# Optimization experiments

Hardware: AMD Instinct MI355X
Metric: run time of the kernel (lower is better)

## Reference

```python
import jax, jax.numpy as jnp
import numpy as np

NUM_ROUTING = 3  # init kwarg num_routing


def setup_inputs() -> dict:
    key = jax.random.key(0)
    k1, k2 = jax.random.split(key)
    # x: [B=128, N=1152 primary caps, C_in=8]
    x = jax.random.normal(k1, (128, 1152, 8), dtype=jnp.float32)
    # dc_w: [capsules_dim=10, num_capsules=1152, C_in=8, C_out=16]
    dc_w = jax.random.normal(k2, (10, 1152, 8, 16), dtype=jnp.float32)
    return {"x": x, "dc_w": dc_w}


def reference(x, dc_w):
    # u = x[None,:,:,None,:] @ dc_w[:,None,:,:,:]  -> [D, B, N, 1, C_out]
    u = jnp.einsum('bni,dnio->dbno', x, dc_w)[:, :, :, None, :]
    b = jnp.zeros_like(u)
    v = None
    for i in range(NUM_ROUTING):  # small fixed routing loop
        c = jax.nn.softmax(b, axis=2)                 # softmax over primary caps
        s = jnp.sum(c * u, axis=2, keepdims=True)     # [D, B, 1, 1, C_out]
        # faithful to source: norm is taken over the (singleton) axis 2,
        # so the squash coefficient is elementwise s^2 / ((1+s^2) * |s|)
        sq = s * s
        coeff = sq / ((1.0 + sq) * jnp.sqrt(sq))
        v = coeff * s
        if i != NUM_ROUTING - 1:
            b = b + jnp.sum(u * v, axis=-1, keepdims=True)  # agreement update
    return v  # [D, B, 1, 1, C_out]
```

## Files before the change

### kernel.cpp

```cpp
#include <hip/hip_runtime.h>
#include <hip/hip_bf16.h>
#include <math.h>

constexpr int NCAPS = 1152;
constexpr int CIN   = 8;
constexpr int COUT  = 16;
constexpr int BATCH = 128;
constexpr int DCAPS = 10;

__global__ __launch_bounds__(256, 1) void u_kernel(
    const float* __restrict__ x,
    const float* __restrict__ w,
    __hip_bfloat16* __restrict__ u)
{
    const int i  = blockIdx.x;
    const int bh = i & 1;
    const int nc = (i >> 1) % 72;
    const int d  = (i >> 1) / 72;

    const int t    = threadIdx.x;
    const int wv   = t >> 6;
    const int lane = t & 63;
    const int oq   = lane & 3;
    const int nl   = lane >> 2;
    const int n    = nc * 16 + nl;
    const int b0   = bh * 64 + wv * 16;

    const float* wr = w + ((size_t)(d * NCAPS + n)) * (CIN * COUT) + oq * 4;
    float4 W[CIN];
    #pragma unroll
    for (int ii = 0; ii < CIN; ++ii)
        W[ii] = *(const float4*)(wr + ii * COUT);

    const float* xp = x + ((size_t)b0 * NCAPS + n) * CIN;
    __hip_bfloat16* up = u + ((size_t)(d * BATCH + b0) * NCAPS + n) * COUT + oq * 4;

    #pragma unroll
    for (int bi = 0; bi < 16; ++bi) {
        const float4* xr = (const float4*)(xp + (size_t)bi * NCAPS * CIN);
        float4 xa = xr[0], xc = xr[1];
        float xs[CIN] = {xa.x, xa.y, xa.z, xa.w, xc.x, xc.y, xc.z, xc.w};
        float4 acc = {0.f, 0.f, 0.f, 0.f};
        #pragma unroll
        for (int ii = 0; ii < CIN; ++ii) {
            acc.x = fmaf(xs[ii], W[ii].x, acc.x);
            acc.y = fmaf(xs[ii], W[ii].y, acc.y);
            acc.z = fmaf(xs[ii], W[ii].z, acc.z);
            acc.w = fmaf(xs[ii], W[ii].w, acc.w);
        }
        union { unsigned short us[4]; uint2 v; } pk;
        pk.us[0] = __bfloat16_as_ushort(__float2bfloat16(acc.x));
        pk.us[1] = __bfloat16_as_ushort(__float2bfloat16(acc.y));
        pk.us[2] = __bfloat16_as_ushort(__float2bfloat16(acc.z));
        pk.us[3] = __bfloat16_as_ushort(__float2bfloat16(acc.w));
        *(uint2*)(up + (size_t)bi * NCAPS * COUT) = pk.v;
    }
}

constexpr int BNT  = 256;
constexpr int BWAV = BNT / 64;
constexpr int JPT  = 9;

__device__ __forceinline__ void unpack8(const uint4 pv, float* f) {
    f[0] = __uint_as_float(pv.x << 16);
    f[1] = __uint_as_float(pv.x & 0xffff0000u);
    f[2] = __uint_as_float(pv.y << 16);
    f[3] = __uint_as_float(pv.y & 0xffff0000u);
    f[4] = __uint_as_float(pv.z << 16);
    f[5] = __uint_as_float(pv.z & 0xffff0000u);
    f[6] = __uint_as_float(pv.w << 16);
    f[7] = __uint_as_float(pv.w & 0xffff0000u);
}

__global__ __launch_bounds__(BNT, 1) void routing_kernel(
    const __hip_bfloat16* __restrict__ u,
    float* __restrict__ out)
{
    __shared__ float red[BWAV][COUT];
    __shared__ float zred[BWAV];

    const int i = blockIdx.x;
    const int d = i >> 7;
    const int b = i & 127;

    const int t    = threadIdx.x;
    const int wave = t >> 6;
    const int lane = t & 63;
    const int oh   = t & 1;
    const int r    = t >> 1;

    const __hip_bfloat16* up =
        u + ((size_t)(d * BATCH + b) * NCAPS) * COUT + oh * 8;

    uint4 upk[JPT];
    #pragma unroll
    for (int j = 0; j < JPT; ++j)
        upk[j] = *(const uint4*)(up + (size_t)(j * 128 + r) * COUT);

    float bb[JPT];
    #pragma unroll
    for (int j = 0; j < JPT; ++j) bb[j] = 0.f;

    #pragma unroll
    for (int it = 0; it < 3; ++it) {
        float p8[8] = {0.f,0.f,0.f,0.f,0.f,0.f,0.f,0.f};
        float z = 0.f;
        if (it == 0) {
            #pragma unroll
            for (int j = 0; j < JPT; ++j) {
                float uf[8]; unpack8(upk[j], uf);
                #pragma unroll
                for (int k = 0; k < 8; ++k) p8[k] += uf[k];
            }
        } else {
            #pragma unroll
            for (int j = 0; j < JPT; ++j) {
                float e = __expf(bb[j] - 20.f);
                z += e;
                float uf[8]; unpack8(upk[j], uf);
                #pragma unroll
                for (int k = 0; k < 8; ++k) p8[k] = fmaf(e, uf[k], p8[k]);
            }
        }
        #pragma unroll
        for (int off = 2; off < 64; off <<= 1) {
            #pragma unroll
            for (int k = 0; k < 8; ++k) p8[k] += __shfl_xor(p8[k], off);
            if (it != 0) z += __shfl_xor(z, off);
        }
        if (lane < 2) {
            #pragma unroll
            for (int k = 0; k < 8; ++k) red[wave][oh * 8 + k] = p8[k];
            if (it != 0 && lane == 0) zred[wave] = z;
        }
        __syncthreads();

        float scale;
        if (it == 0) {
            scale = 1.f / (float)NCAPS;
        } else {
            float Z = zred[0] + zred[1] + zred[2] + zred[3];
            scale = 1.f / Z;
        }
        float vloc[8];
        #pragma unroll
        for (int k = 0; k < 8; ++k) {
            float s = red[0][oh * 8 + k] + red[1][oh * 8 + k]
                    + red[2][oh * 8 + k] + red[3][oh * 8 + k];
            s *= scale;
            vloc[k] = s * fabsf(s) / (1.f + s * s);
        }

        if (it == 2) {
            if (t < 2) {
                float* op = out + ((size_t)d * BATCH + b) * COUT + oh * 8;
                ((float4*)op)[0] = make_float4(vloc[0], vloc[1], vloc[2], vloc[3]);
                ((float4*)op)[1] = make_float4(vloc[4], vloc[5], vloc[6], vloc[7]);
            }
        } else {
            #pragma unroll
            for (int j = 0; j < JPT; ++j) {
                float uf[8]; unpack8(upk[j], uf);
                float dv = 0.f;
                #pragma unroll
                for (int k = 0; k < 8; ++k) dv = fmaf(uf[k], vloc[k], dv);
                dv += __shfl_xor(dv, 1);
                bb[j] += dv;
            }
            __syncthreads();
        }
    }
}

extern "C" void kernel_launch(void* const* d_in, const int* in_sizes, int n_in,
                              void* d_out, int out_size, void* d_ws, size_t ws_size,
                              hipStream_t stream) {
    const float* x = (const float*)d_in[0];
    const float* w = (const float*)d_in[1];
    float* out = (float*)d_out;
    __hip_bfloat16* u = (__hip_bfloat16*)d_ws;

    u_kernel<<<DCAPS * 72 * 2, 256, 0, stream>>>(x, w, u);
    routing_kernel<<<DCAPS * BATCH, BNT, 0, stream>>>(u, out);
}
```

Measured before the change: 88.95 us.

## Remap u_kernel blocks over capsules and double-buffer routing reductions

```diff
diff --git a/kernel.cpp b/kernel.cpp
--- a/kernel.cpp
+++ b/kernel.cpp
@@ -13,18 +13,18 @@
     const float* __restrict__ w,
     __hip_bfloat16* __restrict__ u)
 {
-    const int i  = blockIdx.x;
-    const int bh = i & 1;
-    const int nc = (i >> 1) % 72;
-    const int d  = (i >> 1) / 72;
+    const int i   = blockIdx.x;
+    const int bg  = i & 7;
+    const int k   = i >> 3;
+    const int nc4 = k % 18;
+    const int d   = k / 18;
 
     const int t    = threadIdx.x;
     const int wv   = t >> 6;
     const int lane = t & 63;
     const int oq   = lane & 3;
     const int nl   = lane >> 2;
-    const int n    = nc * 16 + nl;
-    const int b0   = bh * 64 + wv * 16;
+    const int n    = nc4 * 64 + wv * 16 + nl;
 
     const float* wr = w + ((size_t)(d * NCAPS + n)) * (CIN * COUT) + oq * 4;
     float4 W[CIN];
@@ -32,12 +32,13 @@
     for (int ii = 0; ii < CIN; ++ii)
         W[ii] = *(const float4*)(wr + ii * COUT);
 
-    const float* xp = x + ((size_t)b0 * NCAPS + n) * CIN;
-    __hip_bfloat16* up = u + ((size_t)(d * BATCH + b0) * NCAPS + n) * COUT + oq * 4;
+    const float* xp = x + ((size_t)bg * NCAPS + n) * CIN;
+    __hip_bfloat16* up = u + ((size_t)(d * BATCH + bg) * NCAPS + n) * COUT + oq * 4;
 
     #pragma unroll
     for (int bi = 0; bi < 16; ++bi) {
-        const float4* xr = (const float4*)(xp + (size_t)bi * NCAPS * CIN);
+        const float4* xr =
+            (const float4*)(xp + (size_t)bi * 8 * NCAPS * CIN);
         float4 xa = xr[0], xc = xr[1];
         float xs[CIN] = {xa.x, xa.y, xa.z, xa.w, xc.x, xc.y, xc.z, xc.w};
         float4 acc = {0.f, 0.f, 0.f, 0.f};
@@ -53,7 +54,7 @@
         pk.us[1] = __bfloat16_as_ushort(__float2bfloat16(acc.y));
         pk.us[2] = __bfloat16_as_ushort(__float2bfloat16(acc.z));
         pk.us[3] = __bfloat16_as_ushort(__float2bfloat16(acc.w));
-        *(uint2*)(up + (size_t)bi * NCAPS * COUT) = pk.v;
+        *(uint2*)(up + (size_t)bi * 8 * NCAPS * COUT) = pk.v;
     }
 }
 
@@ -76,8 +77,8 @@
     const __hip_bfloat16* __restrict__ u,
     float* __restrict__ out)
 {
-    __shared__ float red[BWAV][COUT];
-    __shared__ float zred[BWAV];
+    __shared__ float red[2][BWAV][COUT];
+    __shared__ float zred[2][BWAV];
 
     const int i = blockIdx.x;
     const int d = i >> 7;
@@ -97,78 +98,87 @@
     for (int j = 0; j < JPT; ++j)
         upk[j] = *(const uint4*)(up + (size_t)(j * 128 + r) * COUT);
 
+    float p8[8] = {0.f,0.f,0.f,0.f,0.f,0.f,0.f,0.f};
+    #pragma unroll
+    for (int j = 0; j < JPT; ++j) {
+        float uf[8]; unpack8(upk[j], uf);
+        #pragma unroll
+        for (int kk = 0; kk < 8; ++kk) p8[kk] += uf[kk];
+    }
+    #pragma unroll
+    for (int off = 2; off < 64; off <<= 1) {
+        #pragma unroll
+        for (int kk = 0; kk < 8; ++kk) p8[kk] += __shfl_xor(p8[kk], off);
+    }
+    if (lane < 2) {
+        #pragma unroll
+        for (int kk = 0; kk < 8; ++kk) red[0][wave][oh * 8 + kk] = p8[kk];
+    }
+    __syncthreads();
+
+    float vloc[8];
+    {
+        const float scale = 1.f / (float)NCAPS;
+        #pragma unroll
+        for (int kk = 0; kk < 8; ++kk) {
+            float s = red[0][0][oh * 8 + kk] + red[0][1][oh * 8 + kk]
+                    + red[0][2][oh * 8 + kk] + red[0][3][oh * 8 + kk];
+            s *= scale;
+            vloc[kk] = s * fabsf(s) / (1.f + s * s);
+        }
+    }
+
     float bb[JPT];
     #pragma unroll
     for (int j = 0; j < JPT; ++j) bb[j] = 0.f;
 
     #pragma unroll
-    for (int it = 0; it < 3; ++it) {
-        float p8[8] = {0.f,0.f,0.f,0.f,0.f,0.f,0.f,0.f};
+    for (int it = 1; it < 3; ++it) {
+        const int buf = it & 1;
+        float q8[8] = {0.f,0.f,0.f,0.f,0.f,0.f,0.f,0.f};
         float z = 0.f;
-        if (it == 0) {
+        #pragma unroll
+        for (int j = 0; j < JPT; ++j) {
+            float uf[8]; unpack8(upk[j], uf);
+            float dv = 0.f;
             #pragma unroll
-            for (int j = 0; j < JPT; ++j) {
-                float uf[8]; unpack8(upk[j], uf);
-                #pragma unroll
-                for (int k = 0; k < 8; ++k) p8[k] += uf[k];
-            }
-        } else {
+            for (int kk = 0; kk < 8; ++kk) dv = fmaf(uf[kk], vloc[kk], dv);
+            dv += __shfl_xor(dv, 1);
+            bb[j] += dv;
+            float e = __expf(bb[j] - 20.f);
+            z += e;
             #pragma unroll
-            for (int j = 0; j < JPT; ++j) {
-                float e = __expf(bb[j] - 20.f);
-                z += e;
-                float uf[8]; unpack8(upk[j], uf);
-                #pragma unroll
-                for (int k = 0; k < 8; ++k) p8[k] = fmaf(e, uf[k], p8[k]);
-            }
+            for (int kk = 0; kk < 8; ++kk) q8[kk] = fmaf(e, uf[kk], q8[kk]);
         }
         #pragma unroll
         for (int off = 2; off < 64; off <<= 1) {
             #pragma unroll
-            for (int k = 0; k < 8; ++k) p8[k] += __shfl_xor(p8[k], off);
-            if (it != 0) z += __shfl_xor(z, off);
+            for (int kk = 0; kk < 8; ++kk) q8[kk] += __shfl_xor(q8[kk], off);
+            z += __shfl_xor(z, off);
         }
         if (lane < 2) {
             #pragma unroll
-            for (int k = 0; k < 8; ++k) red[wave][oh * 8 + k] = p8[k];
-            if (it != 0 && lane == 0) zred[wave] = z;
+            for (int kk = 0; kk < 8; ++kk) red[buf][wave][oh * 8 + kk] = q8[kk];
+            if (lane == 0) zred[buf][wave] = z;
         }
         __syncthreads();
 
-        float scale;
-        if (it == 0) {
-            scale = 1.f / (float)NCAPS;
-        } else {
-            float Z = zred[0] + zred[1] + zred[2] + zred[3];
-            scale = 1.f / Z;
+        const float Z = zred[buf][0] + zred[buf][1]
+                      + zred[buf][2] + zred[buf][3];
+        const float scale = 1.f / Z;
+        #pragma unroll
+        for (int kk = 0; kk < 8; ++kk) {
+            float s = red[buf][0][oh * 8 + kk] + red[buf][1][oh * 8 + kk]
+                    + red[buf][2][oh * 8 + kk] + red[buf][3][oh * 8 + kk];
+            s *= scale;
+            vloc[kk] = s * fabsf(s) / (1.f + s * s);
         }
-        float vloc[8];
-        #pragma unroll
-        for (int k = 0; k < 8; ++k) {
-            float s = red[0][oh * 8 + k] + red[1][oh * 8 + k]
-                    + red[2][oh * 8 + k] + red[3][oh * 8 + k];
-            s *= scale;
-            vloc[k] = s * fabsf(s) / (1.f + s * s);
-        }
+    }
 
-        if (it == 2) {
-            if (t < 2) {
-                float* op = out + ((size_t)d * BATCH + b) * COUT + oh * 8;
-                ((float4*)op)[0] = make_float4(vloc[0], vloc[1], vloc[2], vloc[3]);
-                ((float4*)op)[1] = make_float4(vloc[4], vloc[5], vloc[6], vloc[7]);
-            }
-        } else {
-            #pragma unroll
-            for (int j = 0; j < JPT; ++j) {
-                float uf[8]; unpack8(upk[j], uf);
-                float dv = 0.f;
-                #pragma unroll
-                for (int k = 0; k < 8; ++k) dv = fmaf(uf[k], vloc[k], dv);
-                dv += __shfl_xor(dv, 1);
-                bb[j] += dv;
-            }
-            __syncthreads();
-        }
+    if (t < 2) {
+        float* op = out + ((size_t)d * BATCH + b) * COUT + oh * 8;
+        ((float4*)op)[0] = make_float4(vloc[0], vloc[1], vloc[2], vloc[3]);
+        ((float4*)op)[1] = make_float4(vloc[4], vloc[5], vloc[6], vloc[7]);
     }
 }
 
@@ -180,6 +190,6 @@
     float* out = (float*)d_out;
     __hip_bfloat16* u = (__hip_bfloat16*)d_ws;
 
-    u_kernel<<<DCAPS * 72 * 2, 256, 0, stream>>>(x, w, u);
+    u_kernel<<<DCAPS * 18 * 8, 256, 0, stream>>>(x, w, u);
     routing_kernel<<<DCAPS * BATCH, BNT, 0, stream>>>(u, out);
 }
```

Result: slower. 91.67 us (+3.0%).
